# Performance work log

Hardware: AMD Instinct MI355X
Metric: run time of the kernel (lower is better)

Reference implementation:

```python
import jax, jax.numpy as jnp
import numpy as np

K = 3        # kernel size
PAD = 1      # padding
G = 8        # deform_groups


def conv2d(x, w, b):
    y = jax.lax.conv_general_dilated(x, w, (1, 1), ((PAD, PAD), (PAD, PAD)),
                                     dimension_numbers=('NCHW', 'OIHW', 'NCHW'))
    return y + b[None, :, None, None]


def deform_conv(feat, offset, w, b):
    # feat: [B,C,H,W]; offset: [B, G*K*K*2, H, W] (mmcv layout: per group, per kernel pos, (dy,dx))
    B, C, H, W = feat.shape
    Cg = C // G
    KK = K * K
    off = offset.reshape(B, G, KK, 2, H, W)
    dy, dx = off[:, :, :, 0], off[:, :, :, 1]                      # [B,G,KK,H,W]
    kh = (jnp.arange(KK) // K).astype(feat.dtype)
    kw = (jnp.arange(KK) % K).astype(feat.dtype)
    hh = jnp.arange(H, dtype=feat.dtype)
    ww = jnp.arange(W, dtype=feat.dtype)
    ys = hh[None, None, None, :, None] - PAD + kh[None, None, :, None, None] + dy
    xs = ww[None, None, None, None, :] - PAD + kw[None, None, :, None, None] + dx
    y0 = jnp.floor(ys)
    x0 = jnp.floor(xs)
    wy = (ys - y0)[:, :, None]                                     # [B,G,1,KK,H,W]
    wx = (xs - x0)[:, :, None]
    y0i = y0.astype(jnp.int32)
    x0i = x0.astype(jnp.int32)
    feat_flat = feat.reshape(B, G, Cg, H * W)

    def gather(yi, xi):
        valid = ((yi >= 0) & (yi < H) & (xi >= 0) & (xi < W)).astype(feat.dtype)
        lin = (jnp.clip(yi, 0, H - 1) * W + jnp.clip(xi, 0, W - 1)).astype(jnp.int32)
        lin = lin.reshape(B, G, KK * H * W)
        v = jax.vmap(jax.vmap(lambda f, i: f[:, i]))(feat_flat, lin)  # [B,G,Cg,KK*H*W]
        return v.reshape(B, G, Cg, KK, H, W) * valid[:, :, None]

    v00 = gather(y0i, x0i)
    v01 = gather(y0i, x0i + 1)
    v10 = gather(y0i + 1, x0i)
    v11 = gather(y0i + 1, x0i + 1)
    samp = (v00 * (1 - wy) * (1 - wx) + v01 * (1 - wy) * wx
            + v10 * wy * (1 - wx) + v11 * wy * wx)                 # [B,G,Cg,KK,H,W]
    wg = w.reshape(w.shape[0], G, Cg, KK)                          # [Cout,G,Cg,KK]
    out = jnp.einsum('ogck,bgckhw->bohw', wg, samp)
    return out + b[None, :, None, None]


def setup_inputs() -> dict:
    key = jax.random.key(0)
    k1, k2, k3 = jax.random.split(key, 3)
    B, T, C, H, W = 1, 5, 64, 96, 96
    x = jax.random.normal(k1, (B, T, C, H, W), dtype=jnp.float32)
    # offset conv: 2C -> G*2*K*K; small scale so sampled offsets stay local
    w_off = jax.random.normal(k2, (G * 2 * K * K, 2 * C, K, K), dtype=jnp.float32) * 0.01
    b_off = jnp.zeros((G * 2 * K * K,), dtype=jnp.float32)
    w_dcn = jax.random.normal(k3, (C, C, K, K), dtype=jnp.float32) * (1.0 / np.sqrt(C * K * K))
    b_dcn = jnp.zeros((C,), dtype=jnp.float32)
    return {"x": x, "w_off": w_off, "b_off": b_off, "w_dcn": w_dcn, "b_dcn": b_dcn}


def reference(x, w_off, b_off, w_dcn, b_dcn):
    B, T, C, H, W = x.shape
    center = x[:, T // 2]
    feats = []
    for i in range(T):
        if i == T // 2:
            feats.append(center)
        else:
            neig = x[:, i]
            offset = conv2d(jnp.concatenate([neig, center], axis=1), w_off, b_off)
            feats.append(deform_conv(neig, offset, w_dcn, b_dcn))
    return jnp.stack(feats, axis=1)
```

## Files before the change

kernel.cpp:

```cpp
#include <hip/hip_runtime.h>
#include <hip/hip_bf16.h>

#define HWN 9216
#define PLN (64 * HWN)
#define SLDE 584

typedef __attribute__((ext_vector_type(8))) short bf16x8;
typedef __attribute__((ext_vector_type(4))) float f32x4;

__device__ __forceinline__ unsigned short f2bf(float v) {
    __hip_bfloat16 h = __float2bfloat16(v);
    return __builtin_bit_cast(unsigned short, h);
}
__device__ __forceinline__ float bf2f(unsigned short b) {
    union { unsigned u; float f; } cv; cv.u = ((unsigned)b) << 16;
    return cv.f;
}

__global__ __launch_bounds__(256) void xprep_kernel(
    const float* __restrict__ x, const float* __restrict__ w_dcn,
    const float* __restrict__ w_off, unsigned short* __restrict__ xt,
    unsigned short* __restrict__ wbf, unsigned short* __restrict__ wcbf,
    float* __restrict__ out)
{
    const int t = blockIdx.y;
    const int tid = threadIdx.x;
    if (t == 5) {
        for (int idx = blockIdx.x * 256 + tid; idx < 64 * 576 + 2 * 144 * 576;
             idx += 144 * 256) {
            if (idx < 64 * 576) {
                int o = idx / 576, c = idx % 576;
                int g = c / 72, rem = c % 72, k = rem >> 3, cg = rem & 7;
                wbf[idx] = f2bf(w_dcn[o * 576 + (g * 8 + cg) * 9 + k]);
            } else {
                int i2 = idx - 64 * 576;
                int s = i2 / (144 * 576);
                int o = (i2 / 576) % 144;
                int kk = i2 % 576;
                int g = kk / 72, rem = kk % 72, k = rem >> 3, cg = rem & 7;
                wcbf[i2] = f2bf(w_off[(size_t)o * 1152
                                      + (size_t)(s * 64 + g * 8 + cg) * 9 + k]);
            }
        }
        return;
    }
    const int p0 = blockIdx.x * 64;
    __shared__ unsigned short tile[64][72];
    const float* in = x + (size_t)t * PLN;
    const bool isC = (t == 2);
    for (int idx = tid; idx < 4096; idx += 256) {
        int c = idx >> 6, p = idx & 63;
        float v = in[(size_t)c * HWN + p0 + p];
        tile[p][c] = f2bf(v);
        if (isC) out[(size_t)2 * PLN + (size_t)c * HWN + p0 + p] = v;
    }
    __syncthreads();
    unsigned short* xo = xt + ((size_t)t * HWN + p0) * 64;
    for (int task = tid; task < 512; task += 256) {
        int p = task >> 3, cb = task & 7;
        *reinterpret_cast<bf16x8*>(xo + p * 64 + cb * 8) =
            *reinterpret_cast<const bf16x8*>(&tile[p][cb * 8]);
    }
}

__global__ __launch_bounds__(576, 2) void conv_center_kernel(
    const unsigned short* __restrict__ xt,
    const unsigned short* __restrict__ wcbf,
    float* __restrict__ wsC)
{
    const int p0 = blockIdx.x * 32;
    const int tid = threadIdx.x;
    const int w = tid >> 6, l = tid & 63;
    const int lr = l & 15, lg = l >> 4;

    __shared__ unsigned short smp[32 * SLDE];

    {
        const unsigned short* xb = xt + (size_t)2 * HWN * 64;
        const bf16x8 bz = {0,0,0,0,0,0,0,0};
        bf16x8 stg[4]; int dst[4];
        #pragma unroll
        for (int i = 0; i < 4; ++i) {
            const int tsk = i * 576 + tid;
            const int g = tsk & 7, pl = (tsk >> 3) & 31, k = tsk >> 8;
            const int p = p0 + pl;
            const int y = p / 96, xx = p - y * 96;
            const int r = k / 3, d = k - 3 * (k / 3);
            const int yy = y + r - 1, xw = xx + d - 1;
            const bool valid = (yy >= 0) & (yy < 96) & (xw >= 0) & (xw < 96);
            const int lin = min(max(yy, 0), 95) * 96 + min(max(xw, 0), 95);
            bf16x8 v = *reinterpret_cast<const bf16x8*>(xb + (size_t)lin * 64 + g * 8);
            stg[i] = valid ? v : bz;
            dst[i] = pl * SLDE + g * 72 + k * 8;
        }
        #pragma unroll
        for (int i = 0; i < 4; ++i)
            *reinterpret_cast<bf16x8*>(smp + dst[i]) = stg[i];
    }
    __syncthreads();

    const unsigned short* wp = wcbf + (size_t)1 * 144 * 576
                               + (size_t)(w * 16 + lr) * 576 + lg * 8;
    bf16x8 afr[18];
    #pragma unroll
    for (int ss = 0; ss < 18; ++ss)
        afr[ss] = *reinterpret_cast<const bf16x8*>(wp + ss * 32);

    f32x4 acc[2] = {{0,0,0,0},{0,0,0,0}};
    #pragma unroll
    for (int pt = 0; pt < 2; ++pt) {
        const unsigned short* brow = smp + (pt * 16 + lr) * SLDE + lg * 8;
        #pragma unroll
        for (int ss = 0; ss < 18; ++ss) {
            bf16x8 b = *reinterpret_cast<const bf16x8*>(brow + ss * 32);
            acc[pt] = __builtin_amdgcn_mfma_f32_16x16x32_bf16(afr[ss], b, acc[pt], 0, 0, 0);
        }
    }
    #pragma unroll
    for (int pt = 0; pt < 2; ++pt) {
        const int px = p0 + pt * 16 + lr;
        #pragma unroll
        for (int r = 0; r < 4; ++r) {
            const int o = w * 16 + lg * 4 + r;
            wsC[(size_t)o * HWN + px] = acc[pt][r];
        }
    }
}

__global__ __launch_bounds__(576, 2) void conv_neig_kernel(
    const unsigned short* __restrict__ xt,
    const unsigned short* __restrict__ wcbf,
    const float* __restrict__ b_off,
    const float* __restrict__ wsC,
    float* __restrict__ ofs)
{
    const int f = blockIdx.y;
    const int t = f < 2 ? f : f + 1;
    const int p0 = blockIdx.x * 64;
    const int tid = threadIdx.x;
    const int w = tid >> 6, l = tid & 63;
    const int lr = l & 15, lg = l >> 4;

    __shared__ unsigned short smp[64 * SLDE];

    float wpre[4][4], bpre[4];
    #pragma unroll
    for (int r = 0; r < 4; ++r) {
        const int o = w * 16 + lg * 4 + r;
        bpre[r] = b_off[o];
        #pragma unroll
        for (int pt = 0; pt < 4; ++pt)
            wpre[pt][r] = wsC[(size_t)o * HWN + p0 + pt * 16 + lr];
    }

    {
        const unsigned short* xb = xt + (size_t)t * HWN * 64;
        const bf16x8 bz = {0,0,0,0,0,0,0,0};
        bf16x8 stg[8]; int dst[8];
        #pragma unroll
        for (int i = 0; i < 8; ++i) {
            const int tsk = i * 576 + tid;
            const int g = tsk & 7, pl = (tsk >> 3) & 63, k = tsk >> 9;
            const int p = p0 + pl;
            const int y = p / 96, xx = p - y * 96;
            const int r = k / 3, d = k - 3 * (k / 3);
            const int yy = y + r - 1, xw = xx + d - 1;
            const bool valid = (yy >= 0) & (yy < 96) & (xw >= 0) & (xw < 96);
            const int lin = min(max(yy, 0), 95) * 96 + min(max(xw, 0), 95);
            bf16x8 v = *reinterpret_cast<const bf16x8*>(xb + (size_t)lin * 64 + g * 8);
            stg[i] = valid ? v : bz;
            dst[i] = pl * SLDE + g * 72 + k * 8;
        }
        #pragma unroll
        for (int i = 0; i < 8; ++i)
            *reinterpret_cast<bf16x8*>(smp + dst[i]) = stg[i];
    }
    __syncthreads();

    const unsigned short* wp = wcbf + (size_t)(w * 16 + lr) * 576 + lg * 8;
    bf16x8 afr[18];
    #pragma unroll
    for (int ss = 0; ss < 18; ++ss)
        afr[ss] = *reinterpret_cast<const bf16x8*>(wp + ss * 32);

    f32x4 acc[4] = {{0,0,0,0},{0,0,0,0},{0,0,0,0},{0,0,0,0}};
    #pragma unroll
    for (int pt = 0; pt < 4; ++pt) {
        const unsigned short* brow = smp + (pt * 16 + lr) * SLDE + lg * 8;
        #pragma unroll
        for (int ss = 0; ss < 18; ++ss) {
            bf16x8 b = *reinterpret_cast<const bf16x8*>(brow + ss * 32);
            acc[pt] = __builtin_amdgcn_mfma_f32_16x16x32_bf16(afr[ss], b, acc[pt], 0, 0, 0);
        }
    }

    float* of = ofs + (size_t)f * 144 * HWN;
    #pragma unroll
    for (int pt = 0; pt < 4; ++pt) {
        const int px = p0 + pt * 16 + lr;
        #pragma unroll
        for (int r = 0; r < 4; ++r) {
            const int o = w * 16 + lg * 4 + r;
            of[(size_t)o * HWN + px] = acc[pt][r] + wpre[pt][r] + bpre[r];
        }
    }
}

__global__ __launch_bounds__(256, 4) void deform_kernel(
    const unsigned short* __restrict__ xt,
    const float* __restrict__ ofs,
    const unsigned short* __restrict__ wbf,
    const float* __restrict__ b_dcn,
    float* __restrict__ out)
{
    const int f = blockIdx.y;
    const int t = f < 2 ? f : f + 1;
    const int p0 = blockIdx.x * 32;
    const int tid = threadIdx.x;

    __shared__ unsigned short smp[32 * SLDE];

    float bpre[4];
    {
        const int o0p = (tid >> 6) * 16 + ((tid & 63) >> 4) * 4;
        #pragma unroll
        for (int r = 0; r < 4; ++r) bpre[r] = b_dcn[o0p + r];
    }

    {
        const int g = tid >> 5, pl = tid & 31;
        const int p = p0 + pl;
        const int y = p / 96, xx = p - y * 96;
        const unsigned short* xf = xt + (size_t)t * HWN * 64 + g * 8;
        const float* ob = ofs + (size_t)f * 144 * HWN + (size_t)g * 18 * HWN + p;
        float dy[9], dx[9];
        #pragma unroll
        for (int k = 0; k < 9; ++k) {
            dy[k] = ob[(size_t)(2 * k) * HWN];
            dx[k] = ob[(size_t)(2 * k + 1) * HWN];
        }
        unsigned short* srow = smp + pl * SLDE + g * 72;

        bf16x8 cc[2][4];
        float  ww[2][4];
        auto prep = [&](int k, int buf) {
            const int r = k / 3, d = k - 3 * (k / 3);
            const float ys = (float)(y + r - 1) + dy[k];
            const float xs = (float)(xx + d - 1) + dx[k];
            const float y0f = floorf(ys), x0f = floorf(xs);
            const float wy = ys - y0f, wx = xs - x0f;
            const int y0 = (int)y0f, x0 = (int)x0f;
            const int y1 = y0 + 1, x1 = x0 + 1;
            const bool vy0 = (y0 >= 0) & (y0 < 96);
            const bool vy1 = (y1 >= 0) & (y1 < 96);
            const bool vx0 = (x0 >= 0) & (x0 < 96);
            const bool vx1 = (x1 >= 0) & (x1 < 96);
            const int yc0 = min(max(y0, 0), 95), yc1 = min(max(y1, 0), 95);
            const int xc0 = min(max(x0, 0), 95), xc1 = min(max(x1, 0), 95);
            ww[buf][0] = (vy0 & vx0) ? (1.f - wy) * (1.f - wx) : 0.f;
            ww[buf][1] = (vy0 & vx1) ? (1.f - wy) * wx : 0.f;
            ww[buf][2] = (vy1 & vx0) ? wy * (1.f - wx) : 0.f;
            ww[buf][3] = (vy1 & vx1) ? wy * wx : 0.f;
            cc[buf][0] = *reinterpret_cast<const bf16x8*>(xf + (size_t)(yc0 * 96 + xc0) * 64);
            cc[buf][1] = *reinterpret_cast<const bf16x8*>(xf + (size_t)(yc0 * 96 + xc1) * 64);
            cc[buf][2] = *reinterpret_cast<const bf16x8*>(xf + (size_t)(yc1 * 96 + xc0) * 64);
            cc[buf][3] = *reinterpret_cast<const bf16x8*>(xf + (size_t)(yc1 * 96 + xc1) * 64);
        };

        prep(0, 0);
        #pragma unroll
        for (int k = 0; k < 9; ++k) {
            if (k < 8) prep(k + 1, (k + 1) & 1);
            const int b = k & 1;
            bf16x8 pk;
            #pragma unroll
            for (int ch = 0; ch < 8; ++ch) {
                float v = ww[b][0] * bf2f((unsigned short)cc[b][0][ch]);
                v = fmaf(ww[b][1], bf2f((unsigned short)cc[b][1][ch]), v);
                v = fmaf(ww[b][2], bf2f((unsigned short)cc[b][2][ch]), v);
                v = fmaf(ww[b][3], bf2f((unsigned short)cc[b][3][ch]), v);
                pk[ch] = (short)f2bf(v);
            }
            *reinterpret_cast<bf16x8*>(srow + k * 8) = pk;
        }
    }
    __syncthreads();

    const int w = tid >> 6;
    const int l = tid & 63;
    const int o0 = w * 16;
    const int lr = l & 15, lg = l >> 4;

    bf16x8 afr[18];
    const unsigned short* wrow = wbf + (size_t)(o0 + lr) * 576 + lg * 8;
    #pragma unroll
    for (int s = 0; s < 18; ++s)
        afr[s] = *reinterpret_cast<const bf16x8*>(wrow + s * 32);

    f32x4 acc0 = {0.f, 0.f, 0.f, 0.f}, acc1 = {0.f, 0.f, 0.f, 0.f};
    const unsigned short* brow0 = smp + lr * SLDE + lg * 8;
    const unsigned short* brow1 = brow0 + 16 * SLDE;
    #pragma unroll
    for (int s = 0; s < 18; ++s) {
        bf16x8 b0 = *reinterpret_cast<const bf16x8*>(brow0 + s * 32);
        bf16x8 b1 = *reinterpret_cast<const bf16x8*>(brow1 + s * 32);
        acc0 = __builtin_amdgcn_mfma_f32_16x16x32_bf16(afr[s], b0, acc0, 0, 0, 0);
        acc1 = __builtin_amdgcn_mfma_f32_16x16x32_bf16(afr[s], b1, acc1, 0, 0, 0);
    }

    float* op = out + (size_t)t * PLN + p0;
    #pragma unroll
    for (int r = 0; r < 4; ++r) {
        const int o = o0 + lg * 4 + r;
        op[(size_t)o * HWN + lr] = acc0[r] + bpre[r];
        op[(size_t)o * HWN + 16 + lr] = acc1[r] + bpre[r];
    }
}

extern "C" void kernel_launch(void* const* d_in, const int* in_sizes, int n_in,
                              void* d_out, int out_size, void* d_ws, size_t ws_size,
                              hipStream_t stream) {
    const float* x     = (const float*)d_in[0];
    const float* w_off = (const float*)d_in[1];
    const float* b_off = (const float*)d_in[2];
    const float* w_dcn = (const float*)d_in[3];
    const float* b_dcn = (const float*)d_in[4];
    float* out = (float*)d_out;

    float* ofs          = (float*)d_ws;
    unsigned short* xt  = (unsigned short*)(ofs + (size_t)4 * 144 * HWN);
    unsigned short* wbf = xt + (size_t)5 * HWN * 64;
    unsigned short* wcbf = wbf + (size_t)64 * 576;
    float* wsC = (float*)(wcbf + (size_t)2 * 144 * 576);

    xprep_kernel<<<dim3(144, 6), 256, 0, stream>>>(x, w_dcn, w_off, xt, wbf, wcbf, out);

    conv_center_kernel<<<288, 576, 0, stream>>>(xt, wcbf, wsC);

    conv_neig_kernel<<<dim3(144, 4), 576, 0, stream>>>(xt, wcbf, b_off, wsC, ofs);

    deform_kernel<<<dim3(288, 4), 256, 0, stream>>>(xt, ofs, wbf, b_dcn, out);
}
```

Baseline: 82.37 us.

## Store offset and center-conv buffers pixel-major for vectorized access

Switches the intermediate wsC and offset buffers from channel-major [144][HW] to pixel-major [HW][144]. The MFMA accumulators are written as one float4 per lane, and the deform kernel reads (dy,dx) pairs as float2. The aim is fewer store and load instructions. The cost is less coalescing across lanes, since consecutive pixels now sit 576 bytes apart instead of being contiguous.

Result: no change. 82.74 us (+0.4%).

```diff
diff --git a/kernel.cpp b/kernel.cpp
--- a/kernel.cpp
+++ b/kernel.cpp
@@ -116,14 +116,11 @@
             acc[pt] = __builtin_amdgcn_mfma_f32_16x16x32_bf16(afr[ss], b, acc[pt], 0, 0, 0);
         }
     }
+    const int ob = w * 16 + lg * 4;
     #pragma unroll
     for (int pt = 0; pt < 2; ++pt) {
         const int px = p0 + pt * 16 + lr;
-        #pragma unroll
-        for (int r = 0; r < 4; ++r) {
-            const int o = w * 16 + lg * 4 + r;
-            wsC[(size_t)o * HWN + px] = acc[pt][r];
-        }
+        *reinterpret_cast<f32x4*>(wsC + (size_t)px * 144 + ob) = acc[pt];
     }
 }
 
@@ -140,18 +137,16 @@
     const int tid = threadIdx.x;
     const int w = tid >> 6, l = tid & 63;
     const int lr = l & 15, lg = l >> 4;
+    const int ob = w * 16 + lg * 4;
 
     __shared__ unsigned short smp[64 * SLDE];
 
-    float wpre[4][4], bpre[4];
-    #pragma unroll
-    for (int r = 0; r < 4; ++r) {
-        const int o = w * 16 + lg * 4 + r;
-        bpre[r] = b_off[o];
-        #pragma unroll
-        for (int pt = 0; pt < 4; ++pt)
-            wpre[pt][r] = wsC[(size_t)o * HWN + p0 + pt * 16 + lr];
-    }
+    f32x4 bpre = *reinterpret_cast<const f32x4*>(b_off + ob);
+    f32x4 wpre[4];
+    #pragma unroll
+    for (int pt = 0; pt < 4; ++pt)
+        wpre[pt] = *reinterpret_cast<const f32x4*>(
+            wsC + (size_t)(p0 + pt * 16 + lr) * 144 + ob);
 
     {
         const unsigned short* xb = xt + (size_t)t * HWN * 64;
@@ -194,15 +189,12 @@
         }
     }
 
-    float* of = ofs + (size_t)f * 144 * HWN;
+    float* of = ofs + (size_t)f * HWN * 144;
     #pragma unroll
     for (int pt = 0; pt < 4; ++pt) {
         const int px = p0 + pt * 16 + lr;
-        #pragma unroll
-        for (int r = 0; r < 4; ++r) {
-            const int o = w * 16 + lg * 4 + r;
-            of[(size_t)o * HWN + px] = acc[pt][r] + wpre[pt][r] + bpre[r];
-        }
+        f32x4 v = acc[pt] + wpre[pt] + bpre;
+        *reinterpret_cast<f32x4*>(of + (size_t)px * 144 + ob) = v;
     }
 }
 
@@ -232,12 +224,13 @@
         const int p = p0 + pl;
         const int y = p / 96, xx = p - y * 96;
         const unsigned short* xf = xt + (size_t)t * HWN * 64 + g * 8;
-        const float* ob = ofs + (size_t)f * 144 * HWN + (size_t)g * 18 * HWN + p;
+        const float* obp = ofs + ((size_t)f * HWN + p) * 144 + g * 18;
         float dy[9], dx[9];
         #pragma unroll
         for (int k = 0; k < 9; ++k) {
-            dy[k] = ob[(size_t)(2 * k) * HWN];
-            dx[k] = ob[(size_t)(2 * k + 1) * HWN];
+            float2 dd = *reinterpret_cast<const float2*>(obp + 2 * k);
+            dy[k] = dd.x;
+            dx[k] = dd.y;
         }
         unsigned short* srow = smp + pl * SLDE + g * 72;
 
```
